# Kernel tuning notes

Measured on AMD Instinct MI355X. Metric: run time of the kernel, lower is better.

## Reference

```python
import jax, jax.numpy as jnp
import numpy as np

N, T, K = 64, 256, 4
MODS = ["linguistic", "acoustic", "image"]
DIMS = {"linguistic": 300, "acoustic": 88, "image": 128}
HID = {"linguistic": 300, "acoustic": 64, "image": 128}
TOTAL_H = sum(HID[m] for m in MODS)  # 492


def _uniform(k, shape, s):
    return jax.random.uniform(k, shape, jnp.float32, -s, s)


def setup_inputs() -> dict:
    key = jax.random.key(0)
    ks = iter(jax.random.split(key, 64))
    inp = {}
    for mod in MODS:
        D, H = DIMS[mod], HID[mod]
        inp[f"x_{mod}"] = jax.random.normal(next(ks), (N, T, K, D), jnp.float32)
        inp[f"mask_{mod}"] = jax.random.randint(next(ks), (N, T, K), 0, 2).astype(bool)
        s = 1.0 / np.sqrt(H)
        inp[f"Wih_{mod}"] = _uniform(next(ks), (4 * H, D), s)
        inp[f"Whh_{mod}"] = _uniform(next(ks), (4 * H, H), s)
        inp[f"bih_{mod}"] = _uniform(next(ks), (4 * H,), s)
        inp[f"bhh_{mod}"] = _uniform(next(ks), (4 * H,), s)
    inp["seq_length"] = jax.random.randint(next(ks), (N,), 1, T + 1)
    inp["lstm_masks"] = jax.random.uniform(next(ks), (N, T, 1), jnp.float32)
    s1 = 1.0 / np.sqrt(TOTAL_H)
    inp["fuse_W1"] = _uniform(next(ks), (256, TOTAL_H), s1)
    inp["fuse_b1"] = _uniform(next(ks), (256,), s1)
    s2 = 1.0 / np.sqrt(256)
    inp["fuse_W2"] = _uniform(next(ks), (1, 256), s2)
    inp["fuse_b2"] = _uniform(next(ks), (1,), s2)
    return inp


def _lstm_cell(x, h, c, Wih, Whh, bih, bhh):
    # torch.nn.LSTMCell gate order: i, f, g, o
    z = x @ Wih.T + bih + h @ Whh.T + bhh
    i, f, g, o = jnp.split(z, 4, axis=-1)
    c2 = jax.nn.sigmoid(f) * c + jax.nn.sigmoid(i) * jnp.tanh(g)
    return jax.nn.sigmoid(o) * jnp.tanh(c2), c2


def _run_mod(x, mask, seq_len, Wih, Whh, bih, bhh):
    # x: [N,T,K,D], mask: [N,T,K] bool, seq_len: [N]
    n, t, k, d = x.shape
    hdim = Whh.shape[1]

    def step(carry, inp):
        h, c = carry
        xt, mt, ti = inp  # xt [N,K,D], mt [N,K]

        def inner(hc, ik):
            h0, c0 = hc
            xk, mk = ik  # [N,D], [N]
            h1, c1 = _lstm_cell(xk, h0, c0, Wih, Whh, bih, bhh)
            mk = mk[:, None]
            return (jnp.where(mk, h1, h0), jnp.where(mk, c1, c0)), None

        (h2, c2), _ = jax.lax.scan(inner, (h, c), (jnp.swapaxes(xt, 0, 1), mt.T))
        avail = mt.any(axis=1)[:, None]        # modality present at this step
        active = (ti < seq_len)[:, None]       # sequence not yet finished
        h_new = jnp.where(active & avail, h2, jnp.where(active, h, 0.0))
        c_new = jnp.where(active & avail, c2, jnp.where(active, c, 0.0))
        return (h_new, c_new), h_new

    h0 = jnp.zeros((n, hdim), x.dtype)
    c0 = jnp.zeros((n, hdim), x.dtype)
    _, hs = jax.lax.scan(
        step, (h0, c0),
        (jnp.swapaxes(x, 0, 1), jnp.swapaxes(mask, 0, 1), jnp.arange(t)))
    # FAITHFUL to original: torch.stack -> [T,N,H] then .reshape(n,t,H) with NO transpose
    return hs.reshape(n, t, hdim)


def reference(x_linguistic, mask_linguistic, Wih_linguistic, Whh_linguistic, bih_linguistic, bhh_linguistic,
              x_acoustic, mask_acoustic, Wih_acoustic, Whh_acoustic, bih_acoustic, bhh_acoustic,
              x_image, mask_image, Wih_image, Whh_image, bih_image, bhh_image,
              seq_length, lstm_masks, fuse_W1, fuse_b1, fuse_W2, fuse_b2):
    hs_l = _run_mod(x_linguistic, mask_linguistic, seq_length, Wih_linguistic, Whh_linguistic, bih_linguistic, bhh_linguistic)
    hs_a = _run_mod(x_acoustic, mask_acoustic, seq_length, Wih_acoustic, Whh_acoustic, bih_acoustic, bhh_acoustic)
    hs_i = _run_mod(x_image, mask_image, seq_length, Wih_image, Whh_image, bih_image, bhh_image)
    fused = jnp.concatenate([hs_l, hs_a, hs_i], axis=2)  # [N,T,492]
    h = fused @ fuse_W1.T + fuse_b1   # Dropout is identity in eval mode
    out = h @ fuse_W2.T + fuse_b2     # [N,T,1]
    return out * lstm_masks
```

## Files before the change

### kernel.cpp

```cpp
#include <hip/hip_runtime.h>
#include <hip/hip_bf16.h>
#include <stdint.h>

#define N_ 64
#define T_ 256
#define K_ 4

#define DL 300
#define HL 300
#define H4L 1200
#define DA 88
#define HA 64
#define H4A 256
#define DI 128
#define HI 128
#define H4I 512
#define DLP 320
#define DAP 96
#define DIP 128

typedef __hip_bfloat16 bf16;
typedef __attribute__((ext_vector_type(8))) short bf16x8;
typedef __attribute__((ext_vector_type(4))) float f32x4;

__device__ __forceinline__ float sigf(float x) { return 1.0f / (1.0f + expf(-x)); }

__device__ __forceinline__ unsigned pk2(float lo, float hi) {
    bf16 a = __float2bfloat16(lo), b = __float2bfloat16(hi);
    return (unsigned)*(unsigned short*)&a | ((unsigned)*(unsigned short*)&b << 16);
}
__device__ __forceinline__ float uplo(unsigned u) { return __uint_as_float(u << 16); }
__device__ __forceinline__ float uphi(unsigned u) { return __uint_as_float(u & 0xFFFF0000u); }

__device__ __forceinline__ int read_mask(const void* m, size_t idx, int mode) {
    if (mode == 0) return ((const int*)m)[idx];
    if (mode == 1) return (int)((const unsigned char*)m)[idx];
    return ((const float*)m)[idx] != 0.0f;
}

__global__ void mask_mode_detect(const unsigned int* __restrict__ m, int* __restrict__ modep) {
    __shared__ unsigned int f[2];
    if (threadIdx.x == 0) { f[0] = 0u; f[1] = 0u; }
    __syncthreads();
    unsigned int gt1 = 0, f32one = 0;
    for (int i = threadIdx.x; i < 4096; i += 256) {
        const unsigned int v = m[i];
        if (v > 1u) gt1 = 1u;
        if (v == 0x3F800000u) f32one = 1u;
    }
    if (gt1) atomicOr(&f[0], 1u);
    if (f32one) atomicOr(&f[1], 1u);
    __syncthreads();
    if (threadIdx.x == 0) modep[0] = f[0] ? (f[1] ? 2 : 1) : 0;
}

__global__ void prep_w3(const float* __restrict__ WL, const float* __restrict__ WA,
                        const float* __restrict__ WI,
                        unsigned short* __restrict__ pL, unsigned short* __restrict__ pA,
                        unsigned short* __restrict__ pI)
{
    const int i = blockIdx.x * 256 + threadIdx.x;
    if (i < H4L * DLP) {
        const int r = i / DLP, d = i - r * DLP;
        bf16 v = __float2bfloat16(d < DL ? WL[(size_t)r * DL + d] : 0.0f);
        pL[i] = *(unsigned short*)&v;
    }
    if (i < H4A * DAP) {
        const int r = i / DAP, d = i - r * DAP;
        bf16 v = __float2bfloat16(d < DA ? WA[(size_t)r * DA + d] : 0.0f);
        pA[i] = *(unsigned short*)&v;
    }
    if (i < H4I * DIP) {
        const int r = i / DIP, d = i - r * DIP;
        bf16 v = __float2bfloat16(WI[(size_t)r * DI + d]);
        pI[i] = *(unsigned short*)&v;
    }
}

__global__ __launch_bounds__(256) void gemm_xz3(
    const float* __restrict__ XL, const unsigned short* __restrict__ WL,
    const float* __restrict__ biL, const float* __restrict__ bhL, bf16* __restrict__ ZL,
    const float* __restrict__ XA, const unsigned short* __restrict__ WA,
    const float* __restrict__ biA, const float* __restrict__ bhA, bf16* __restrict__ ZA,
    const float* __restrict__ XI, const unsigned short* __restrict__ WI,
    const float* __restrict__ biI, const float* __restrict__ bhI, bf16* __restrict__ ZI,
    const int* __restrict__ seqlen, int Tc, int t0)
{
    __shared__ __align__(16) unsigned short Xs[64 * 40];
    __shared__ __align__(16) unsigned short Ws[64 * 40];
    const int z = blockIdx.z;
    const float* X; const unsigned short* W; const float* bih; const float* bhh; bf16* XZ;
    int D, Dp, H4;
    if (z == 0)      { X = XL; W = WL; bih = biL; bhh = bhL; XZ = ZL; D = DL; Dp = DLP; H4 = H4L; }
    else if (z == 1) { X = XA; W = WA; bih = biA; bhh = bhA; XZ = ZA; D = DA; Dp = DAP; H4 = H4A; }
    else             { X = XI; W = WI; bih = biI; bhh = bhI; XZ = ZI; D = DI; Dp = DIP; H4 = H4I; }

    const int j0 = blockIdx.x * 64;
    if (j0 >= H4) return;

    const int tid = threadIdx.x;
    const int m0 = blockIdx.y * 64;
    const int Tc4 = Tc * 4;

    int act = 0;
    if (tid < 64) {
        const int rr = m0 + tid;
        const int n = rr / Tc4;
        const int ttt = (rr % Tc4) >> 2;
        act = (t0 + ttt) < seqlen[n];
    }
    if (!__syncthreads_or(act)) return;

    const int srow = tid >> 2;
    const int sq = tid & 3;
    const int rr = m0 + srow;
    const int n = rr / Tc4;
    const int ttt = (rr % Tc4) >> 2;
    const int kk_ = rr & 3;
    const float* xrow = X + ((size_t)((n * T_ + t0 + ttt) * 4 + kk_)) * D;
    const int wcol = j0 + srow;
    const bool wvalid = wcol < H4;
    const unsigned short* wrow = W + (size_t)(wvalid ? wcol : 0) * Dp;

    const int lane = tid & 63;
    const int wv = tid >> 6;
    const int fr = lane & 15;
    const int fk = (lane >> 4) * 8;

    f32x4 acc[4] = {{0,0,0,0},{0,0,0,0},{0,0,0,0},{0,0,0,0}};

    const int nks = Dp >> 5;
    for (int ks = 0; ks < nks; ++ks) {
        const int d0 = ks * 32 + sq * 8;
        float xf[8];
        if (d0 + 7 < D) {
            const float4 a0 = *(const float4*)(xrow + d0);
            const float4 a1 = *(const float4*)(xrow + d0 + 4);
            xf[0]=a0.x; xf[1]=a0.y; xf[2]=a0.z; xf[3]=a0.w;
            xf[4]=a1.x; xf[5]=a1.y; xf[6]=a1.z; xf[7]=a1.w;
        } else {
#pragma unroll
            for (int e = 0; e < 8; ++e) {
                const int d = d0 + e;
                xf[e] = (d < D) ? xrow[d] : 0.0f;
            }
        }
        union { unsigned short u[8]; uint4 v; } px;
#pragma unroll
        for (int e = 0; e < 8; ++e) {
            bf16 hx = __float2bfloat16(xf[e]);
            px.u[e] = *(unsigned short*)&hx;
        }
        uint4 pwv = make_uint4(0u, 0u, 0u, 0u);
        if (wvalid) pwv = *(const uint4*)&wrow[d0];
        __syncthreads();
        *(uint4*)&Xs[srow * 40 + sq * 8] = px.v;
        *(uint4*)&Ws[srow * 40 + sq * 8] = pwv;
        __syncthreads();
        const bf16x8 a = *(const bf16x8*)&Xs[(wv * 16 + fr) * 40 + fk];
#pragma unroll
        for (int c = 0; c < 4; ++c) {
            const bf16x8 b = *(const bf16x8*)&Ws[(c * 16 + fr) * 40 + fk];
            acc[c] = __builtin_amdgcn_mfma_f32_16x16x32_bf16(a, b, acc[c], 0, 0, 0);
        }
    }
#pragma unroll
    for (int c = 0; c < 4; ++c) {
        const int col = j0 + c * 16 + fr;
        if (col < H4) {
            const float bias = bih[col] + bhh[col];
#pragma unroll
            for (int rg = 0; rg < 4; ++rg) {
                const int row = m0 + wv * 16 + (lane >> 4) * 4 + rg;
                XZ[(size_t)row * H4 + col] = __float2bfloat16(acc[c][rg] + bias);
            }
        }
    }
}

__global__ __launch_bounds__(512, 1) void recur_all(
    const float* __restrict__ WhhL, const float* __restrict__ WhhA,
    const float* __restrict__ WhhI,
    const void* __restrict__ mL, const void* __restrict__ mA, const void* __restrict__ mI,
    const int* __restrict__ modep,
    const int* __restrict__ seqlen,
    const float* __restrict__ wbuf,
    const bf16* __restrict__ xzL, const bf16* __restrict__ xzA, const bf16* __restrict__ xzI,
    float* __restrict__ psumL, float* __restrict__ psumA, float* __restrict__ psumI,
    float* __restrict__ hcL, float* __restrict__ hcA, float* __restrict__ hcI,
    float* __restrict__ hpub,
    unsigned int* __restrict__ cnt,
    int Tc, int t0)
{
    __shared__ float h_s[304];
    __shared__ float c_s[80];
    __shared__ float zp_s[8 * 308];
    __shared__ float zr_s[304];
    __shared__ float wb_s[304];
    __shared__ __align__(16) float h2_s[128];
    __shared__ __align__(16) float c2_s[128];
    __shared__ __align__(16) float z2_s[512];
    __shared__ float wb2_s[128];
    const int tid = threadIdx.x;
    const int mode = modep[0];

    if (blockIdx.x < 4 * N_) {
        const int xcd = blockIdx.x & 7;
        const int idx = blockIdx.x >> 3;
        const int n = xcd * 8 + (idx >> 2);
        const int b = idx & 3;
        const int hb = 75 * b;
        const int seqn = seqlen[n];

        const int chunk = tid & 7;
        const int rb = tid >> 3;
        const int cj = chunk * 38;
        unsigned w[5][19];
#pragma unroll
        for (int s = 0; s < 5; ++s) {
            const int lr = rb + 64 * s;
            const bool rv = (lr < 300);
            const int gl = rv ? (lr / 75) : 0;
            const int i  = rv ? (lr - gl * 75) : 0;
            const float* wp = WhhL + ((size_t)(gl * 300 + hb + i)) * 300;
#pragma unroll
            for (int j = 0; j < 19; ++j) {
                const int c0 = cj + 2 * j;
                const float lo = (rv && c0 < 300) ? wp[c0] : 0.0f;
                const float hi = (rv && c0 + 1 < 300) ? wp[c0 + 1] : 0.0f;
                w[s][j] = pk2(lo, hi);
            }
        }
        int xoff = 0;
        if (tid < 300) {
            const int gl = tid / 75;
            xoff = gl * 300 + hb + (tid - gl * 75);
        }
        for (int r = tid; r < 304; r += 512) {
            if (t0 == 0 || r >= 300) h_s[r] = 0.0f;
            else h_s[r] = hcL[n * 600 + r];
            wb_s[r] = (r < 300) ? wbuf[r] : 0.0f;
        }
        if (tid < 75) c_s[tid] = (t0 == 0) ? 0.0f : hcL[n * 600 + 300 + hb + tid];
        __syncthreads();

        unsigned int serial = 0;
        unsigned int* const cntn = &cnt[n];
        float* const hp = hpub + (size_t)n * 608;

#pragma unroll 1
        for (int tt = 0; tt < Tc; ++tt) {
            const int t = t0 + tt;
            if (t >= seqn) {
                if (b == 0 && tid == 0) psumL[(size_t)n * T_ + t] = 0.0f;
                continue;
            }
            const size_t mbase = (size_t)(n * T_ + t) * 4;
            const bf16* xzt = xzL + ((size_t)((n * Tc + tt) * 4)) * 1200;
#pragma unroll 1
            for (int k = 0; k < 4; ++k) {
                if (!read_mask(mL, mbase + k, mode)) continue;
                const int par = (int)(serial & 1u);
                float a0 = 0.f, a1 = 0.f, a2 = 0.f, a3 = 0.f, a4 = 0.f;
#pragma unroll
                for (int j = 0; j < 19; ++j) {
                    const float2 hv = *(const float2*)&h_s[cj + 2 * j];
                    const unsigned u0 = w[0][j], u1 = w[1][j], u2 = w[2][j],
                                   u3 = w[3][j], u4 = w[4][j];
                    a0 += uplo(u0) * hv.x + uphi(u0) * hv.y;
                    a1 += uplo(u1) * hv.x + uphi(u1) * hv.y;
                    a2 += uplo(u2) * hv.x + uphi(u2) * hv.y;
                    a3 += uplo(u3) * hv.x + uphi(u3) * hv.y;
                    a4 += uplo(u4) * hv.x + uphi(u4) * hv.y;
                }
                zp_s[chunk * 308 + rb]       = a0;
                zp_s[chunk * 308 + rb + 64]  = a1;
                zp_s[chunk * 308 + rb + 128] = a2;
                zp_s[chunk * 308 + rb + 192] = a3;
                if (rb < 44) zp_s[chunk * 308 + rb + 256] = a4;
                __syncthreads();
                if (tid < 300) {
                    float zv = __bfloat162float(xzt[k * 1200 + xoff]);
#pragma unroll
                    for (int c = 0; c < 8; ++c) zv += zp_s[c * 308 + tid];
                    zr_s[tid] = zv;
                }
                __syncthreads();
                if (tid < 75) {
                    const float zi = zr_s[tid];
                    const float zf = zr_s[75 + tid];
                    const float zg = zr_s[150 + tid];
                    const float zo = zr_s[225 + tid];
                    const float cc = sigf(zf) * c_s[tid] + sigf(zi) * tanhf(zg);
                    c_s[tid] = cc;
                    const float hh = sigf(zo) * tanhf(cc);
                    __hip_atomic_store(&hp[par * 304 + hb + tid], hh,
                                       __ATOMIC_RELAXED, __HIP_MEMORY_SCOPE_AGENT);
                }
                __syncthreads();
                if (tid == 0) {
                    __hip_atomic_fetch_add(cntn, 1u, __ATOMIC_RELEASE, __HIP_MEMORY_SCOPE_AGENT);
                    const unsigned int target = 4u * (serial + 1u);
                    unsigned int v = __hip_atomic_load(cntn, __ATOMIC_ACQUIRE, __HIP_MEMORY_SCOPE_AGENT);
                    long guard = 0;
                    while (v < target && guard < (1L << 24)) {
                        __builtin_amdgcn_s_sleep(1);
                        v = __hip_atomic_load(cntn, __ATOMIC_ACQUIRE, __HIP_MEMORY_SCOPE_AGENT);
                        ++guard;
                    }
                }
                __syncthreads();
                if (tid < 300)
                    h_s[tid] = __hip_atomic_load(&hp[par * 304 + tid],
                                                 __ATOMIC_RELAXED, __HIP_MEMORY_SCOPE_AGENT);
                __syncthreads();
                ++serial;
            }
            if (b == 0 && tid < 64) {
                float v = 0.0f;
                for (int r = tid; r < 300; r += 64) v += wb_s[r] * h_s[r];
#pragma unroll
                for (int off = 32; off; off >>= 1) v += __shfl_down(v, off, 64);
                if (tid == 0) psumL[(size_t)n * T_ + t] = v;
            }
        }
        if (tid < 75) {
            hcL[n * 600 + hb + tid] = h_s[hb + tid];
            hcL[n * 600 + 300 + hb + tid] = c_s[tid];
        }
    } else if (blockIdx.x < 4 * N_ + N_) {
        const int n = blockIdx.x - 4 * N_;
        const int seqn = seqlen[n];
        unsigned w[64];
        {
            const float4* wp = (const float4*)(WhhI + (size_t)tid * 128);
#pragma unroll
            for (int jj = 0; jj < 32; ++jj) {
                const float4 v = wp[jj];
                w[2 * jj]     = pk2(v.x, v.y);
                w[2 * jj + 1] = pk2(v.z, v.w);
            }
        }
        if (tid < 128) {
            if (t0 == 0) { h2_s[tid] = 0.0f; c2_s[tid] = 0.0f; }
            else { h2_s[tid] = hcI[n * 256 + tid]; c2_s[tid] = hcI[n * 256 + 128 + tid]; }
            wb2_s[tid] = wbuf[364 + tid];
        }
        __syncthreads();
#pragma unroll 1
        for (int tt = 0; tt < Tc; ++tt) {
            const int t = t0 + tt;
            if (t >= seqn) {
                if (tid == 0) psumI[(size_t)n * T_ + t] = 0.0f;
                continue;
            }
            const size_t xbase = ((size_t)((n * Tc + tt) * 4)) * 512;
            const size_t mbase = (size_t)(n * T_ + t) * 4;
#pragma unroll 1
            for (int k = 0; k < 4; ++k) {
                if (!read_mask(mI, mbase + k, mode)) continue;
                float acc = __bfloat162float(xzI[xbase + k * 512 + tid]);
                const float2* hp2 = (const float2*)h2_s;
#pragma unroll
                for (int jj = 0; jj < 64; ++jj) {
                    const float2 hv = hp2[jj];
                    const unsigned u = w[jj];
                    acc += uplo(u) * hv.x + uphi(u) * hv.y;
                }
                z2_s[tid] = acc;
                __syncthreads();
                if (tid < 128) {
                    const float zi = z2_s[tid], zf = z2_s[128 + tid];
                    const float zg = z2_s[256 + tid], zo = z2_s[384 + tid];
                    const float cc = sigf(zf) * c2_s[tid] + sigf(zi) * tanhf(zg);
                    c2_s[tid] = cc;
                    h2_s[tid] = sigf(zo) * tanhf(cc);
                }
                __syncthreads();
            }
            if (tid < 64) {
                float v = wb2_s[tid] * h2_s[tid] + wb2_s[tid + 64] * h2_s[tid + 64];
#pragma unroll
                for (int off = 32; off; off >>= 1) v += __shfl_down(v, off, 64);
                if (tid == 0) psumI[(size_t)n * T_ + t] = v;
            }
        }
        if (tid < 128) { hcI[n * 256 + tid] = h2_s[tid]; hcI[n * 256 + 128 + tid] = c2_s[tid]; }
    } else {
        const int n = blockIdx.x - 5 * N_;
        const int seqn = seqlen[n];
        unsigned w[32];
        if (tid < 256) {
            const float4* wp = (const float4*)(WhhA + (size_t)tid * 64);
#pragma unroll
            for (int jj = 0; jj < 16; ++jj) {
                const float4 v = wp[jj];
                w[2 * jj]     = pk2(v.x, v.y);
                w[2 * jj + 1] = pk2(v.z, v.w);
            }
        }
        if (tid < 64) {
            if (t0 == 0) { h2_s[tid] = 0.0f; c2_s[tid] = 0.0f; }
            else { h2_s[tid] = hcA[n * 128 + tid]; c2_s[tid] = hcA[n * 128 + 64 + tid]; }
            wb2_s[tid] = wbuf[300 + tid];
        }
        __syncthreads();
#pragma unroll 1
        for (int tt = 0; tt < Tc; ++tt) {
            const int t = t0 + tt;
            if (t >= seqn) {
                if (tid == 0) psumA[(size_t)n * T_ + t] = 0.0f;
                continue;
            }
            const size_t xbase = ((size_t)((n * Tc + tt) * 4)) * 256;
            const size_t mbase = (size_t)(n * T_ + t) * 4;
#pragma unroll 1
            for (int k = 0; k < 4; ++k) {
                if (!read_mask(mA, mbase + k, mode)) continue;
                if (tid < 256) {
                    float acc = __bfloat162float(xzA[xbase + k * 256 + tid]);
                    const float2* hp2 = (const float2*)h2_s;
#pragma unroll
                    for (int jj = 0; jj < 32; ++jj) {
                        const float2 hv = hp2[jj];
                        const unsigned u = w[jj];
                        acc += uplo(u) * hv.x + uphi(u) * hv.y;
                    }
                    z2_s[tid] = acc;
                }
                __syncthreads();
                if (tid < 64) {
                    const float zi = z2_s[tid], zf = z2_s[64 + tid];
                    const float zg = z2_s[128 + tid], zo = z2_s[192 + tid];
                    const float cc = sigf(zf) * c2_s[tid] + sigf(zi) * tanhf(zg);
                    c2_s[tid] = cc;
                    h2_s[tid] = sigf(zo) * tanhf(cc);
                }
                __syncthreads();
            }
            if (tid < 64) {
                float v = wb2_s[tid] * h2_s[tid];
#pragma unroll
                for (int off = 32; off; off >>= 1) v += __shfl_down(v, off, 64);
                if (tid == 0) psumA[(size_t)n * T_ + t] = v;
            }
        }
        if (tid < 64) { hcA[n * 128 + tid] = h2_s[tid]; hcA[n * 128 + 64 + tid] = c2_s[tid]; }
    }
}

__global__ void wprep(const float* __restrict__ W1, const float* __restrict__ b1,
                      const float* __restrict__ W2, const float* __restrict__ b2,
                      float* __restrict__ wbuf)
{
    const int j = threadIdx.x;
    if (j < 492) {
        float a = 0.0f;
        for (int r = 0; r < 256; ++r) a += W2[r] * W1[r * 492 + j];
        wbuf[j] = a;
    } else if (j == 492) {
        float a = 0.0f;
        for (int r = 0; r < 256; ++r) a += W2[r] * b1[r];
        wbuf[500] = a + b2[0];
    }
}

__global__ void out_combine(const float* __restrict__ wbuf,
                            const float* __restrict__ pL, const float* __restrict__ pA,
                            const float* __restrict__ pI,
                            const float* __restrict__ lmask, float* __restrict__ out)
{
    const int i = blockIdx.x;
    const int j = threadIdx.x;
    const int nn = j & 63;
    const int tt = i * 4 + (j >> 6);
    const size_t src = (size_t)nn * T_ + tt;
    const size_t nt = (size_t)i * T_ + j;
    out[nt] = (pL[src] + pA[src] + pI[src] + wbuf[500]) * lmask[nt];
}

extern "C" void kernel_launch(void* const* d_in, const int* in_sizes, int n_in,
                              void* d_out, int out_size, void* d_ws, size_t ws_size,
                              hipStream_t stream)
{
    (void)in_sizes; (void)n_in;
    const float* xL   = (const float*)d_in[0];
    const void*  mL   = d_in[1];
    const float* WihL = (const float*)d_in[2];
    const float* WhhL = (const float*)d_in[3];
    const float* bihL = (const float*)d_in[4];
    const float* bhhL = (const float*)d_in[5];
    const float* xA   = (const float*)d_in[6];
    const void*  mA   = d_in[7];
    const float* WihA = (const float*)d_in[8];
    const float* WhhA = (const float*)d_in[9];
    const float* bihA = (const float*)d_in[10];
    const float* bhhA = (const float*)d_in[11];
    const float* xI   = (const float*)d_in[12];
    const void*  mI   = d_in[13];
    const float* WihI = (const float*)d_in[14];
    const float* WhhI = (const float*)d_in[15];
    const float* bihI = (const float*)d_in[16];
    const float* bhhI = (const float*)d_in[17];
    const int*   seqlen = (const int*)d_in[18];
    const float* lmask  = (const float*)d_in[19];
    const float* W1 = (const float*)d_in[20];
    const float* b1 = (const float*)d_in[21];
    const float* W2 = (const float*)d_in[22];
    const float* b2 = (const float*)d_in[23];
    float* out = (float*)d_out;

    char* base = (char*)d_ws;
    size_t off = 0;
    auto take = [&](size_t bytes) -> char* {
        char* p = base + off;
        off += (bytes + 63) & ~(size_t)63;
        return p;
    };
    unsigned int* cnt = (unsigned int*)take(64 * 64 * sizeof(unsigned int));
    int*   modep = (int*)take(64);
    float* wbuf  = (float*)take(512 * sizeof(float));
    float* hcL   = (float*)take((size_t)N_ * 2 * HL * sizeof(float));
    float* hcA   = (float*)take((size_t)N_ * 2 * HA * sizeof(float));
    float* hcI   = (float*)take((size_t)N_ * 2 * HI * sizeof(float));
    float* hpub  = (float*)take((size_t)N_ * 2 * 304 * sizeof(float));
    float* psumL = (float*)take((size_t)N_ * T_ * sizeof(float));
    float* psumA = (float*)take((size_t)N_ * T_ * sizeof(float));
    float* psumI = (float*)take((size_t)N_ * T_ * sizeof(float));
    unsigned short* wpkL = (unsigned short*)take((size_t)H4L * DLP * sizeof(unsigned short));
    unsigned short* wpkA = (unsigned short*)take((size_t)H4A * DAP * sizeof(unsigned short));
    unsigned short* wpkI = (unsigned short*)take((size_t)H4I * DIP * sizeof(unsigned short));

    const size_t xz_per_tc = (size_t)N_ * K_ * (H4L + H4A + H4I) * sizeof(bf16);
    int Tc = T_;
    while (Tc > 1 && off + (size_t)Tc * xz_per_tc + 256 > ws_size) Tc >>= 1;
    if (off + (size_t)Tc * xz_per_tc + 256 > ws_size) {
        hipMemsetAsync(d_out, 0, (size_t)out_size * sizeof(float), stream);
        return;
    }
    if (Tc > 64) Tc = 64;
    bf16* xzL = (bf16*)take((size_t)N_ * Tc * K_ * H4L * sizeof(bf16));
    bf16* xzA = (bf16*)take((size_t)N_ * Tc * K_ * H4A * sizeof(bf16));
    bf16* xzI = (bf16*)take((size_t)N_ * Tc * K_ * H4I * sizeof(bf16));

    const int nchunks = T_ / Tc;
    hipMemsetAsync(cnt, 0, (size_t)nchunks * 64 * sizeof(unsigned int), stream);
    mask_mode_detect<<<1, 256, 0, stream>>>((const unsigned int*)mL, modep);
    wprep<<<1, 512, 0, stream>>>(W1, b1, W2, b2, wbuf);
    prep_w3<<<(H4L * DLP + 255) / 256, 256, 0, stream>>>(WihL, WihA, WihI, wpkL, wpkA, wpkI);

    const int My = (N_ * Tc * K_) / 64;
    for (int c = 0; c < nchunks; ++c) {
        const int t0 = c * Tc;
        gemm_xz3<<<dim3((H4L + 63) / 64, My, 3), 256, 0, stream>>>(
            xL, wpkL, bihL, bhhL, xzL,
            xA, wpkA, bihA, bhhA, xzA,
            xI, wpkI, bihI, bhhI, xzI,
            seqlen, Tc, t0);
        recur_all<<<6 * N_, 512, 0, stream>>>(
            WhhL, WhhA, WhhI, mL, mA, mI, modep, seqlen, wbuf,
            xzL, xzA, xzI, psumL, psumA, psumI,
            hcL, hcA, hcI, hpub, cnt + (size_t)c * 64, Tc, t0);
    }
    out_combine<<<N_, T_, 0, stream>>>(wbuf, psumL, psumA, psumI, lmask, out);
}
```

Before: 3.959 ms.

## Fuse input-projection GEMM into recurrence kernel and overlap next chunk's GEMM

Merges the separate input-projection GEMM and recurrence kernels into one 'mega' kernel. Each launch runs the recurrence for the current time chunk on 6*N blocks, while extra blocks compute the next chunk's projections into a double buffer. The goal is to hide GEMM time behind the latency-bound serial recurrence and to cut launch count. The cost is double the xz workspace, and the GEMM blocks may compete for CUs with the recurrence blocks, which spin-wait on each other.

```diff
diff --git a/kernel.cpp b/kernel.cpp
--- a/kernel.cpp
+++ b/kernel.cpp
@@ -18,6 +18,10 @@
 #define DLP 320
 #define DAP 96
 #define DIP 128
+#define XT_L 19
+#define XT_A 4
+#define XT_I 8
+#define XT_ALL 31
 
 typedef __hip_bfloat16 bf16;
 typedef __attribute__((ext_vector_type(8))) short bf16x8;
@@ -74,378 +78,6 @@
         const int r = i / DIP, d = i - r * DIP;
         bf16 v = __float2bfloat16(WI[(size_t)r * DI + d]);
         pI[i] = *(unsigned short*)&v;
-    }
-}
-
-__global__ __launch_bounds__(256) void gemm_xz3(
-    const float* __restrict__ XL, const unsigned short* __restrict__ WL,
-    const float* __restrict__ biL, const float* __restrict__ bhL, bf16* __restrict__ ZL,
-    const float* __restrict__ XA, const unsigned short* __restrict__ WA,
-    const float* __restrict__ biA, const float* __restrict__ bhA, bf16* __restrict__ ZA,
-    const float* __restrict__ XI, const unsigned short* __restrict__ WI,
-    const float* __restrict__ biI, const float* __restrict__ bhI, bf16* __restrict__ ZI,
-    const int* __restrict__ seqlen, int Tc, int t0)
-{
-    __shared__ __align__(16) unsigned short Xs[64 * 40];
-    __shared__ __align__(16) unsigned short Ws[64 * 40];
-    const int z = blockIdx.z;
-    const float* X; const unsigned short* W; const float* bih; const float* bhh; bf16* XZ;
-    int D, Dp, H4;
-    if (z == 0)      { X = XL; W = WL; bih = biL; bhh = bhL; XZ = ZL; D = DL; Dp = DLP; H4 = H4L; }
-    else if (z == 1) { X = XA; W = WA; bih = biA; bhh = bhA; XZ = ZA; D = DA; Dp = DAP; H4 = H4A; }
-    else             { X = XI; W = WI; bih = biI; bhh = bhI; XZ = ZI; D = DI; Dp = DIP; H4 = H4I; }
-
-    const int j0 = blockIdx.x * 64;
-    if (j0 >= H4) return;
-
-    const int tid = threadIdx.x;
-    const int m0 = blockIdx.y * 64;
-    const int Tc4 = Tc * 4;
-
-    int act = 0;
-    if (tid < 64) {
-        const int rr = m0 + tid;
-        const int n = rr / Tc4;
-        const int ttt = (rr % Tc4) >> 2;
-        act = (t0 + ttt) < seqlen[n];
-    }
-    if (!__syncthreads_or(act)) return;
-
-    const int srow = tid >> 2;
-    const int sq = tid & 3;
-    const int rr = m0 + srow;
-    const int n = rr / Tc4;
-    const int ttt = (rr % Tc4) >> 2;
-    const int kk_ = rr & 3;
-    const float* xrow = X + ((size_t)((n * T_ + t0 + ttt) * 4 + kk_)) * D;
-    const int wcol = j0 + srow;
-    const bool wvalid = wcol < H4;
-    const unsigned short* wrow = W + (size_t)(wvalid ? wcol : 0) * Dp;
-
-    const int lane = tid & 63;
-    const int wv = tid >> 6;
-    const int fr = lane & 15;
-    const int fk = (lane >> 4) * 8;
-
-    f32x4 acc[4] = {{0,0,0,0},{0,0,0,0},{0,0,0,0},{0,0,0,0}};
-
-    const int nks = Dp >> 5;
-    for (int ks = 0; ks < nks; ++ks) {
-        const int d0 = ks * 32 + sq * 8;
-        float xf[8];
-        if (d0 + 7 < D) {
-            const float4 a0 = *(const float4*)(xrow + d0);
-            const float4 a1 = *(const float4*)(xrow + d0 + 4);
-            xf[0]=a0.x; xf[1]=a0.y; xf[2]=a0.z; xf[3]=a0.w;
-            xf[4]=a1.x; xf[5]=a1.y; xf[6]=a1.z; xf[7]=a1.w;
-        } else {
-#pragma unroll
-            for (int e = 0; e < 8; ++e) {
-                const int d = d0 + e;
-                xf[e] = (d < D) ? xrow[d] : 0.0f;
-            }
-        }
-        union { unsigned short u[8]; uint4 v; } px;
-#pragma unroll
-        for (int e = 0; e < 8; ++e) {
-            bf16 hx = __float2bfloat16(xf[e]);
-            px.u[e] = *(unsigned short*)&hx;
-        }
-        uint4 pwv = make_uint4(0u, 0u, 0u, 0u);
-        if (wvalid) pwv = *(const uint4*)&wrow[d0];
-        __syncthreads();
-        *(uint4*)&Xs[srow * 40 + sq * 8] = px.v;
-        *(uint4*)&Ws[srow * 40 + sq * 8] = pwv;
-        __syncthreads();
-        const bf16x8 a = *(const bf16x8*)&Xs[(wv * 16 + fr) * 40 + fk];
-#pragma unroll
-        for (int c = 0; c < 4; ++c) {
-            const bf16x8 b = *(const bf16x8*)&Ws[(c * 16 + fr) * 40 + fk];
-            acc[c] = __builtin_amdgcn_mfma_f32_16x16x32_bf16(a, b, acc[c], 0, 0, 0);
-        }
-    }
-#pragma unroll
-    for (int c = 0; c < 4; ++c) {
-        const int col = j0 + c * 16 + fr;
-        if (col < H4) {
-            const float bias = bih[col] + bhh[col];
-#pragma unroll
-            for (int rg = 0; rg < 4; ++rg) {
-                const int row = m0 + wv * 16 + (lane >> 4) * 4 + rg;
-                XZ[(size_t)row * H4 + col] = __float2bfloat16(acc[c][rg] + bias);
-            }
-        }
-    }
-}
-
-__global__ __launch_bounds__(512, 1) void recur_all(
-    const float* __restrict__ WhhL, const float* __restrict__ WhhA,
-    const float* __restrict__ WhhI,
-    const void* __restrict__ mL, const void* __restrict__ mA, const void* __restrict__ mI,
-    const int* __restrict__ modep,
-    const int* __restrict__ seqlen,
-    const float* __restrict__ wbuf,
-    const bf16* __restrict__ xzL, const bf16* __restrict__ xzA, const bf16* __restrict__ xzI,
-    float* __restrict__ psumL, float* __restrict__ psumA, float* __restrict__ psumI,
-    float* __restrict__ hcL, float* __restrict__ hcA, float* __restrict__ hcI,
-    float* __restrict__ hpub,
-    unsigned int* __restrict__ cnt,
-    int Tc, int t0)
-{
-    __shared__ float h_s[304];
-    __shared__ float c_s[80];
-    __shared__ float zp_s[8 * 308];
-    __shared__ float zr_s[304];
-    __shared__ float wb_s[304];
-    __shared__ __align__(16) float h2_s[128];
-    __shared__ __align__(16) float c2_s[128];
-    __shared__ __align__(16) float z2_s[512];
-    __shared__ float wb2_s[128];
-    const int tid = threadIdx.x;
-    const int mode = modep[0];
-
-    if (blockIdx.x < 4 * N_) {
-        const int xcd = blockIdx.x & 7;
-        const int idx = blockIdx.x >> 3;
-        const int n = xcd * 8 + (idx >> 2);
-        const int b = idx & 3;
-        const int hb = 75 * b;
-        const int seqn = seqlen[n];
-
-        const int chunk = tid & 7;
-        const int rb = tid >> 3;
-        const int cj = chunk * 38;
-        unsigned w[5][19];
-#pragma unroll
-        for (int s = 0; s < 5; ++s) {
-            const int lr = rb + 64 * s;
-            const bool rv = (lr < 300);
-            const int gl = rv ? (lr / 75) : 0;
-            const int i  = rv ? (lr - gl * 75) : 0;
-            const float* wp = WhhL + ((size_t)(gl * 300 + hb + i)) * 300;
-#pragma unroll
-            for (int j = 0; j < 19; ++j) {
-                const int c0 = cj + 2 * j;
-                const float lo = (rv && c0 < 300) ? wp[c0] : 0.0f;
-                const float hi = (rv && c0 + 1 < 300) ? wp[c0 + 1] : 0.0f;
-                w[s][j] = pk2(lo, hi);
-            }
-        }
-        int xoff = 0;
-        if (tid < 300) {
-            const int gl = tid / 75;
-            xoff = gl * 300 + hb + (tid - gl * 75);
-        }
-        for (int r = tid; r < 304; r += 512) {
-            if (t0 == 0 || r >= 300) h_s[r] = 0.0f;
-            else h_s[r] = hcL[n * 600 + r];
-            wb_s[r] = (r < 300) ? wbuf[r] : 0.0f;
-        }
-        if (tid < 75) c_s[tid] = (t0 == 0) ? 0.0f : hcL[n * 600 + 300 + hb + tid];
-        __syncthreads();
-
-        unsigned int serial = 0;
-        unsigned int* const cntn = &cnt[n];
-        float* const hp = hpub + (size_t)n * 608;
-
-#pragma unroll 1
-        for (int tt = 0; tt < Tc; ++tt) {
-            const int t = t0 + tt;
-            if (t >= seqn) {
-                if (b == 0 && tid == 0) psumL[(size_t)n * T_ + t] = 0.0f;
-                continue;
-            }
-            const size_t mbase = (size_t)(n * T_ + t) * 4;
-            const bf16* xzt = xzL + ((size_t)((n * Tc + tt) * 4)) * 1200;
-#pragma unroll 1
-            for (int k = 0; k < 4; ++k) {
-                if (!read_mask(mL, mbase + k, mode)) continue;
-                const int par = (int)(serial & 1u);
-                float a0 = 0.f, a1 = 0.f, a2 = 0.f, a3 = 0.f, a4 = 0.f;
-#pragma unroll
-                for (int j = 0; j < 19; ++j) {
-                    const float2 hv = *(const float2*)&h_s[cj + 2 * j];
-                    const unsigned u0 = w[0][j], u1 = w[1][j], u2 = w[2][j],
-                                   u3 = w[3][j], u4 = w[4][j];
-                    a0 += uplo(u0) * hv.x + uphi(u0) * hv.y;
-                    a1 += uplo(u1) * hv.x + uphi(u1) * hv.y;
-                    a2 += uplo(u2) * hv.x + uphi(u2) * hv.y;
-                    a3 += uplo(u3) * hv.x + uphi(u3) * hv.y;
-                    a4 += uplo(u4) * hv.x + uphi(u4) * hv.y;
-                }
-                zp_s[chunk * 308 + rb]       = a0;
-                zp_s[chunk * 308 + rb + 64]  = a1;
-                zp_s[chunk * 308 + rb + 128] = a2;
-                zp_s[chunk * 308 + rb + 192] = a3;
-                if (rb < 44) zp_s[chunk * 308 + rb + 256] = a4;
-                __syncthreads();
-                if (tid < 300) {
-                    float zv = __bfloat162float(xzt[k * 1200 + xoff]);
-#pragma unroll
-                    for (int c = 0; c < 8; ++c) zv += zp_s[c * 308 + tid];
-                    zr_s[tid] = zv;
-                }
-                __syncthreads();
-                if (tid < 75) {
-                    const float zi = zr_s[tid];
-                    const float zf = zr_s[75 + tid];
-                    const float zg = zr_s[150 + tid];
-                    const float zo = zr_s[225 + tid];
-                    const float cc = sigf(zf) * c_s[tid] + sigf(zi) * tanhf(zg);
-                    c_s[tid] = cc;
-                    const float hh = sigf(zo) * tanhf(cc);
-                    __hip_atomic_store(&hp[par * 304 + hb + tid], hh,
-                                       __ATOMIC_RELAXED, __HIP_MEMORY_SCOPE_AGENT);
-                }
-                __syncthreads();
-                if (tid == 0) {
-                    __hip_atomic_fetch_add(cntn, 1u, __ATOMIC_RELEASE, __HIP_MEMORY_SCOPE_AGENT);
-                    const unsigned int target = 4u * (serial + 1u);
-                    unsigned int v = __hip_atomic_load(cntn, __ATOMIC_ACQUIRE, __HIP_MEMORY_SCOPE_AGENT);
-                    long guard = 0;
-                    while (v < target && guard < (1L << 24)) {
-                        __builtin_amdgcn_s_sleep(1);
-                        v = __hip_atomic_load(cntn, __ATOMIC_ACQUIRE, __HIP_MEMORY_SCOPE_AGENT);
-                        ++guard;
-                    }
-                }
-                __syncthreads();
-                if (tid < 300)
-                    h_s[tid] = __hip_atomic_load(&hp[par * 304 + tid],
-                                                 __ATOMIC_RELAXED, __HIP_MEMORY_SCOPE_AGENT);
-                __syncthreads();
-                ++serial;
-            }
-            if (b == 0 && tid < 64) {
-                float v = 0.0f;
-                for (int r = tid; r < 300; r += 64) v += wb_s[r] * h_s[r];
-#pragma unroll
-                for (int off = 32; off; off >>= 1) v += __shfl_down(v, off, 64);
-                if (tid == 0) psumL[(size_t)n * T_ + t] = v;
-            }
-        }
-        if (tid < 75) {
-            hcL[n * 600 + hb + tid] = h_s[hb + tid];
-            hcL[n * 600 + 300 + hb + tid] = c_s[tid];
-        }
-    } else if (blockIdx.x < 4 * N_ + N_) {
-        const int n = blockIdx.x - 4 * N_;
-        const int seqn = seqlen[n];
-        unsigned w[64];
-        {
-            const float4* wp = (const float4*)(WhhI + (size_t)tid * 128);
-#pragma unroll
-            for (int jj = 0; jj < 32; ++jj) {
-                const float4 v = wp[jj];
-                w[2 * jj]     = pk2(v.x, v.y);
-                w[2 * jj + 1] = pk2(v.z, v.w);
-            }
-        }
-        if (tid < 128) {
-            if (t0 == 0) { h2_s[tid] = 0.0f; c2_s[tid] = 0.0f; }
-            else { h2_s[tid] = hcI[n * 256 + tid]; c2_s[tid] = hcI[n * 256 + 128 + tid]; }
-            wb2_s[tid] = wbuf[364 + tid];
-        }
-        __syncthreads();
-#pragma unroll 1
-        for (int tt = 0; tt < Tc; ++tt) {
-            const int t = t0 + tt;
-            if (t >= seqn) {
-                if (tid == 0) psumI[(size_t)n * T_ + t] = 0.0f;
-                continue;
-            }
-            const size_t xbase = ((size_t)((n * Tc + tt) * 4)) * 512;
-            const size_t mbase = (size_t)(n * T_ + t) * 4;
-#pragma unroll 1
-            for (int k = 0; k < 4; ++k) {
-                if (!read_mask(mI, mbase + k, mode)) continue;
-                float acc = __bfloat162float(xzI[xbase + k * 512 + tid]);
-                const float2* hp2 = (const float2*)h2_s;
-#pragma unroll
-                for (int jj = 0; jj < 64; ++jj) {
-                    const float2 hv = hp2[jj];
-                    const unsigned u = w[jj];
-                    acc += uplo(u) * hv.x + uphi(u) * hv.y;
-                }
-                z2_s[tid] = acc;
-                __syncthreads();
-                if (tid < 128) {
-                    const float zi = z2_s[tid], zf = z2_s[128 + tid];
-                    const float zg = z2_s[256 + tid], zo = z2_s[384 + tid];
-                    const float cc = sigf(zf) * c2_s[tid] + sigf(zi) * tanhf(zg);
-                    c2_s[tid] = cc;
-                    h2_s[tid] = sigf(zo) * tanhf(cc);
-                }
-                __syncthreads();
-            }
-            if (tid < 64) {
-                float v = wb2_s[tid] * h2_s[tid] + wb2_s[tid + 64] * h2_s[tid + 64];
-#pragma unroll
-                for (int off = 32; off; off >>= 1) v += __shfl_down(v, off, 64);
-                if (tid == 0) psumI[(size_t)n * T_ + t] = v;
-            }
-        }
-        if (tid < 128) { hcI[n * 256 + tid] = h2_s[tid]; hcI[n * 256 + 128 + tid] = c2_s[tid]; }
-    } else {
-        const int n = blockIdx.x - 5 * N_;
-        const int seqn = seqlen[n];
-        unsigned w[32];
-        if (tid < 256) {
-            const float4* wp = (const float4*)(WhhA + (size_t)tid * 64);
-#pragma unroll
-            for (int jj = 0; jj < 16; ++jj) {
-                const float4 v = wp[jj];
-                w[2 * jj]     = pk2(v.x, v.y);
-                w[2 * jj + 1] = pk2(v.z, v.w);
-            }
-        }
-        if (tid < 64) {
-            if (t0 == 0) { h2_s[tid] = 0.0f; c2_s[tid] = 0.0f; }
-            else { h2_s[tid] = hcA[n * 128 + tid]; c2_s[tid] = hcA[n * 128 + 64 + tid]; }
-            wb2_s[tid] = wbuf[300 + tid];
-        }
-        __syncthreads();
-#pragma unroll 1
-        for (int tt = 0; tt < Tc; ++tt) {
-            const int t = t0 + tt;
-            if (t >= seqn) {
-                if (tid == 0) psumA[(size_t)n * T_ + t] = 0.0f;
-                continue;
-            }
-            const size_t xbase = ((size_t)((n * Tc + tt) * 4)) * 256;
-            const size_t mbase = (size_t)(n * T_ + t) * 4;
-#pragma unroll 1
-            for (int k = 0; k < 4; ++k) {
-                if (!read_mask(mA, mbase + k, mode)) continue;
-                if (tid < 256) {
-                    float acc = __bfloat162float(xzA[xbase + k * 256 + tid]);
-                    const float2* hp2 = (const float2*)h2_s;
-#pragma unroll
-                    for (int jj = 0; jj < 32; ++jj) {
-                        const float2 hv = hp2[jj];
-                        const unsigned u = w[jj];
-                        acc += uplo(u) * hv.x + uphi(u) * hv.y;
-                    }
-                    z2_s[tid] = acc;
-                }
-                __syncthreads();
-                if (tid < 64) {
-                    const float zi = z2_s[tid], zf = z2_s[64 + tid];
-                    const float zg = z2_s[128 + tid], zo = z2_s[192 + tid];
-                    const float cc = sigf(zf) * c2_s[tid] + sigf(zi) * tanhf(zg);
-                    c2_s[tid] = cc;
-                    h2_s[tid] = sigf(zo) * tanhf(cc);
-                }
-                __syncthreads();
-            }
-            if (tid < 64) {
-                float v = wb2_s[tid] * h2_s[tid];
-#pragma unroll
-                for (int off = 32; off; off >>= 1) v += __shfl_down(v, off, 64);
-                if (tid == 0) psumA[(size_t)n * T_ + t] = v;
-            }
-        }
-        if (tid < 64) { hcA[n * 128 + tid] = h2_s[tid]; hcA[n * 128 + 64 + tid] = c2_s[tid]; }
     }
 }
 
@@ -462,6 +94,378 @@
         float a = 0.0f;
         for (int r = 0; r < 256; ++r) a += W2[r] * b1[r];
         wbuf[500] = a + b2[0];
+    }
+}
+
+__global__ __launch_bounds__(512, 1) void mega(
+    const float* __restrict__ WhhL, const float* __restrict__ WhhA,
+    const float* __restrict__ WhhI,
+    const void* __restrict__ mL, const void* __restrict__ mA, const void* __restrict__ mI,
+    const int* __restrict__ modep,
+    const int* __restrict__ seqlen,
+    const float* __restrict__ wbuf,
+    const bf16* __restrict__ rxL, const bf16* __restrict__ rxA, const bf16* __restrict__ rxI,
+    float* __restrict__ psumL, float* __restrict__ psumA, float* __restrict__ psumI,
+    float* __restrict__ hcL, float* __restrict__ hcA, float* __restrict__ hcI,
+    float* __restrict__ hpub,
+    unsigned int* __restrict__ cnt,
+    const float* __restrict__ XL, const unsigned short* __restrict__ WpL,
+    const float* __restrict__ biL, const float* __restrict__ bhL, bf16* __restrict__ gzL,
+    const float* __restrict__ XA, const unsigned short* __restrict__ WpA,
+    const float* __restrict__ biA, const float* __restrict__ bhA, bf16* __restrict__ gzA,
+    const float* __restrict__ XI, const unsigned short* __restrict__ WpI,
+    const float* __restrict__ biI, const float* __restrict__ bhI, bf16* __restrict__ gzI,
+    int Tc, int t0, int g_t0, int nRecur)
+{
+    __shared__ float h_s[304];
+    __shared__ float c_s[80];
+    __shared__ float zp_s[8 * 308];
+    __shared__ float zr_s[304];
+    __shared__ float wb_s[304];
+    __shared__ __align__(16) float h2_s[128];
+    __shared__ __align__(16) float c2_s[128];
+    __shared__ __align__(16) float z2_s[512];
+    __shared__ float wb2_s[128];
+    __shared__ __align__(16) unsigned short Xs[128 * 40];
+    __shared__ __align__(16) unsigned short Ws[64 * 40];
+
+    const int tid = threadIdx.x;
+    const int mode = modep[0];
+    const int Tc4 = Tc * 4;
+
+    if ((int)blockIdx.x >= nRecur) {
+        if (g_t0 < 0) return;
+        const int gb = blockIdx.x - nRecur;
+        const int y = gb / XT_ALL;
+        const int rem = gb - y * XT_ALL;
+        const float* X; const unsigned short* W; const float* bih; const float* bhh; bf16* XZ;
+        int D, Dp, H4, xt;
+        if (rem < XT_L)            { xt = rem;          X = XL; W = WpL; bih = biL; bhh = bhL; XZ = gzL; D = DL; Dp = DLP; H4 = H4L; }
+        else if (rem < XT_L + XT_A){ xt = rem - XT_L;   X = XA; W = WpA; bih = biA; bhh = bhA; XZ = gzA; D = DA; Dp = DAP; H4 = H4A; }
+        else                       { xt = rem - XT_L - XT_A; X = XI; W = WpI; bih = biI; bhh = bhI; XZ = gzI; D = DI; Dp = DIP; H4 = H4I; }
+        const int j0 = xt * 64;
+        const int m0 = y * 128;
+
+        int act = 0;
+        if (tid < 128) {
+            const int rr = m0 + tid;
+            const int n = rr / Tc4;
+            const int ttt = (rr % Tc4) >> 2;
+            act = (g_t0 + ttt) < seqlen[n];
+        }
+        if (!__syncthreads_or(act)) return;
+
+        const int srow = tid >> 2;
+        const int sq = tid & 3;
+        const int rr = m0 + srow;
+        const int n = rr / Tc4;
+        const int ttt = (rr % Tc4) >> 2;
+        const int kk_ = rr & 3;
+        const float* xrow = X + ((size_t)((n * T_ + g_t0 + ttt) * 4 + kk_)) * D;
+        const int wsrow = tid >> 2;
+        const int wcol = j0 + wsrow;
+        const bool wvalid = (tid < 256) && (wcol < H4);
+        const unsigned short* wrow = W + (size_t)(wvalid ? wcol : 0) * Dp;
+
+        const int lane = tid & 63;
+        const int wv = tid >> 6;
+        const int fr = lane & 15;
+        const int fk = (lane >> 4) * 8;
+
+        f32x4 acc[4] = {{0,0,0,0},{0,0,0,0},{0,0,0,0},{0,0,0,0}};
+
+        const int nks = Dp >> 5;
+        for (int ks = 0; ks < nks; ++ks) {
+            const int d0 = ks * 32 + sq * 8;
+            float xf[8];
+            if (d0 + 7 < D) {
+                const float4 a0 = *(const float4*)(xrow + d0);
+                const float4 a1 = *(const float4*)(xrow + d0 + 4);
+                xf[0]=a0.x; xf[1]=a0.y; xf[2]=a0.z; xf[3]=a0.w;
+                xf[4]=a1.x; xf[5]=a1.y; xf[6]=a1.z; xf[7]=a1.w;
+            } else {
+#pragma unroll
+                for (int e = 0; e < 8; ++e) {
+                    const int d = d0 + e;
+                    xf[e] = (d < D) ? xrow[d] : 0.0f;
+                }
+            }
+            union { unsigned short u[8]; uint4 v; } px;
+#pragma unroll
+            for (int e = 0; e < 8; ++e) {
+                bf16 hx = __float2bfloat16(xf[e]);
+                px.u[e] = *(unsigned short*)&hx;
+            }
+            uint4 pwv = make_uint4(0u, 0u, 0u, 0u);
+            if (wvalid) pwv = *(const uint4*)&wrow[d0];
+            __syncthreads();
+            *(uint4*)&Xs[srow * 40 + sq * 8] = px.v;
+            if (tid < 256) *(uint4*)&Ws[wsrow * 40 + sq * 8] = pwv;
+            __syncthreads();
+            const bf16x8 a = *(const bf16x8*)&Xs[(wv * 16 + fr) * 40 + fk];
+#pragma unroll
+            for (int c = 0; c < 4; ++c) {
+                const bf16x8 b = *(const bf16x8*)&Ws[(c * 16 + fr) * 40 + fk];
+                acc[c] = __builtin_amdgcn_mfma_f32_16x16x32_bf16(a, b, acc[c], 0, 0, 0);
+            }
+        }
+#pragma unroll
+        for (int c = 0; c < 4; ++c) {
+            const int col = j0 + c * 16 + fr;
+            if (col < H4) {
+                const float bias = bih[col] + bhh[col];
+#pragma unroll
+                for (int rg = 0; rg < 4; ++rg) {
+                    const int row = m0 + wv * 16 + (lane >> 4) * 4 + rg;
+                    XZ[(size_t)row * H4 + col] = __float2bfloat16(acc[c][rg] + bias);
+                }
+            }
+        }
+        return;
+    }
+
+    if (blockIdx.x < 4 * N_) {
+        const int xcd = blockIdx.x & 7;
+        const int idx = blockIdx.x >> 3;
+        const int n = xcd * 8 + (idx >> 2);
+        const int b = idx & 3;
+        const int hb = 75 * b;
+        const int seqn = seqlen[n];
+
+        const int chunk = tid & 7;
+        const int rb = tid >> 3;
+        const int cj = chunk * 38;
+        unsigned w[5][19];
+#pragma unroll
+        for (int s = 0; s < 5; ++s) {
+            const int lr = rb + 64 * s;
+            const bool rv = (lr < 300);
+            const int gl = rv ? (lr / 75) : 0;
+            const int i  = rv ? (lr - gl * 75) : 0;
+            const float* wp = WhhL + ((size_t)(gl * 300 + hb + i)) * 300;
+#pragma unroll
+            for (int j = 0; j < 19; ++j) {
+                const int c0 = cj + 2 * j;
+                const float lo = (rv && c0 < 300) ? wp[c0] : 0.0f;
+                const float hi = (rv && c0 + 1 < 300) ? wp[c0 + 1] : 0.0f;
+                w[s][j] = pk2(lo, hi);
+            }
+        }
+        int xoff = 0;
+        if (tid < 300) {
+            const int gl = tid / 75;
+            xoff = gl * 300 + hb + (tid - gl * 75);
+        }
+        for (int r = tid; r < 304; r += 512) {
+            if (t0 == 0 || r >= 300) h_s[r] = 0.0f;
+            else h_s[r] = hcL[n * 600 + r];
+            wb_s[r] = (r < 300) ? wbuf[r] : 0.0f;
+        }
+        if (tid < 75) c_s[tid] = (t0 == 0) ? 0.0f : hcL[n * 600 + 300 + hb + tid];
+        __syncthreads();
+
+        unsigned int serial = 0;
+        unsigned int* const cntn = &cnt[n];
+        float* const hp = hpub + (size_t)n * 608;
+
+#pragma unroll 1
+        for (int tt = 0; tt < Tc; ++tt) {
+            const int t = t0 + tt;
+            if (t >= seqn) {
+                if (b == 0 && tid == 0) psumL[(size_t)n * T_ + t] = 0.0f;
+                continue;
+            }
+            const size_t mbase = (size_t)(n * T_ + t) * 4;
+            const bf16* xzt = rxL + ((size_t)((n * Tc + tt) * 4)) * 1200;
+#pragma unroll 1
+            for (int k = 0; k < 4; ++k) {
+                if (!read_mask(mL, mbase + k, mode)) continue;
+                const int par = (int)(serial & 1u);
+                float a0 = 0.f, a1 = 0.f, a2 = 0.f, a3 = 0.f, a4 = 0.f;
+#pragma unroll
+                for (int j = 0; j < 19; ++j) {
+                    const float2 hv = *(const float2*)&h_s[cj + 2 * j];
+                    const unsigned u0 = w[0][j], u1 = w[1][j], u2 = w[2][j],
+                                   u3 = w[3][j], u4 = w[4][j];
+                    a0 += uplo(u0) * hv.x + uphi(u0) * hv.y;
+                    a1 += uplo(u1) * hv.x + uphi(u1) * hv.y;
+                    a2 += uplo(u2) * hv.x + uphi(u2) * hv.y;
+                    a3 += uplo(u3) * hv.x + uphi(u3) * hv.y;
+                    a4 += uplo(u4) * hv.x + uphi(u4) * hv.y;
+                }
+                zp_s[chunk * 308 + rb]       = a0;
+                zp_s[chunk * 308 + rb + 64]  = a1;
+                zp_s[chunk * 308 + rb + 128] = a2;
+                zp_s[chunk * 308 + rb + 192] = a3;
+                if (rb < 44) zp_s[chunk * 308 + rb + 256] = a4;
+                __syncthreads();
+                if (tid < 300) {
+                    float zv = __bfloat162float(xzt[k * 1200 + xoff]);
+#pragma unroll
+                    for (int c = 0; c < 8; ++c) zv += zp_s[c * 308 + tid];
+                    zr_s[tid] = zv;
+                }
+                __syncthreads();
+                if (tid < 75) {
+                    const float zi = zr_s[tid];
+                    const float zf = zr_s[75 + tid];
+                    const float zg = zr_s[150 + tid];
+                    const float zo = zr_s[225 + tid];
+                    const float cc = sigf(zf) * c_s[tid] + sigf(zi) * tanhf(zg);
+                    c_s[tid] = cc;
+                    const float hh = sigf(zo) * tanhf(cc);
+                    __hip_atomic_store(&hp[par * 304 + hb + tid], hh,
+                                       __ATOMIC_RELAXED, __HIP_MEMORY_SCOPE_AGENT);
+                }
+                __syncthreads();
+                if (tid == 0) {
+                    __hip_atomic_fetch_add(cntn, 1u, __ATOMIC_RELEASE, __HIP_MEMORY_SCOPE_AGENT);
+                    const unsigned int target = 4u * (serial + 1u);
+                    unsigned int v = __hip_atomic_load(cntn, __ATOMIC_ACQUIRE, __HIP_MEMORY_SCOPE_AGENT);
+                    long guard = 0;
+                    while (v < target && guard < (1L << 22)) {
+                        __builtin_amdgcn_s_sleep(1);
+                        v = __hip_atomic_load(cntn, __ATOMIC_ACQUIRE, __HIP_MEMORY_SCOPE_AGENT);
+                        ++guard;
+                    }
+                }
+                __syncthreads();
+                if (tid < 300)
+                    h_s[tid] = __hip_atomic_load(&hp[par * 304 + tid],
+                                                 __ATOMIC_RELAXED, __HIP_MEMORY_SCOPE_AGENT);
+                __syncthreads();
+                ++serial;
+            }
+            if (b == 0 && tid < 64) {
+                float v = 0.0f;
+                for (int r = tid; r < 300; r += 64) v += wb_s[r] * h_s[r];
+#pragma unroll
+                for (int off = 32; off; off >>= 1) v += __shfl_down(v, off, 64);
+                if (tid == 0) psumL[(size_t)n * T_ + t] = v;
+            }
+        }
+        if (tid < 75) {
+            hcL[n * 600 + hb + tid] = h_s[hb + tid];
+            hcL[n * 600 + 300 + hb + tid] = c_s[tid];
+        }
+    } else if (blockIdx.x < 5 * N_) {
+        const int n = blockIdx.x - 4 * N_;
+        const int seqn = seqlen[n];
+        unsigned w[64];
+        {
+            const float4* wp = (const float4*)(WhhI + (size_t)tid * 128);
+#pragma unroll
+            for (int jj = 0; jj < 32; ++jj) {
+                const float4 v = wp[jj];
+                w[2 * jj]     = pk2(v.x, v.y);
+                w[2 * jj + 1] = pk2(v.z, v.w);
+            }
+        }
+        if (tid < 128) {
+            if (t0 == 0) { h2_s[tid] = 0.0f; c2_s[tid] = 0.0f; }
+            else { h2_s[tid] = hcI[n * 256 + tid]; c2_s[tid] = hcI[n * 256 + 128 + tid]; }
+            wb2_s[tid] = wbuf[364 + tid];
+        }
+        __syncthreads();
+#pragma unroll 1
+        for (int tt = 0; tt < Tc; ++tt) {
+            const int t = t0 + tt;
+            if (t >= seqn) {
+                if (tid == 0) psumI[(size_t)n * T_ + t] = 0.0f;
+                continue;
+            }
+            const size_t xbase = ((size_t)((n * Tc + tt) * 4)) * 512;
+            const size_t mbase = (size_t)(n * T_ + t) * 4;
+#pragma unroll 1
+            for (int k = 0; k < 4; ++k) {
+                if (!read_mask(mI, mbase + k, mode)) continue;
+                float acc = __bfloat162float(rxI[xbase + k * 512 + tid]);
+                const float2* hp2 = (const float2*)h2_s;
+#pragma unroll
+                for (int jj = 0; jj < 64; ++jj) {
+                    const float2 hv = hp2[jj];
+                    const unsigned u = w[jj];
+                    acc += uplo(u) * hv.x + uphi(u) * hv.y;
+                }
+                z2_s[tid] = acc;
+                __syncthreads();
+                if (tid < 128) {
+                    const float zi = z2_s[tid], zf = z2_s[128 + tid];
+                    const float zg = z2_s[256 + tid], zo = z2_s[384 + tid];
+                    const float cc = sigf(zf) * c2_s[tid] + sigf(zi) * tanhf(zg);
+                    c2_s[tid] = cc;
+                    h2_s[tid] = sigf(zo) * tanhf(cc);
+                }
+                __syncthreads();
+            }
+            if (tid < 64) {
+                float v = wb2_s[tid] * h2_s[tid] + wb2_s[tid + 64] * h2_s[tid + 64];
+#pragma unroll
+                for (int off = 32; off; off >>= 1) v += __shfl_down(v, off, 64);
+                if (tid == 0) psumI[(size_t)n * T_ + t] = v;
+            }
+        }
+        if (tid < 128) { hcI[n * 256 + tid] = h2_s[tid]; hcI[n * 256 + 128 + tid] = c2_s[tid]; }
+    } else {
+        const int n = blockIdx.x - 5 * N_;
+        const int seqn = seqlen[n];
+        unsigned w[32];
+        if (tid < 256) {
+            const float4* wp = (const float4*)(WhhA + (size_t)tid * 64);
+#pragma unroll
+            for (int jj = 0; jj < 16; ++jj) {
+                const float4 v = wp[jj];
+                w[2 * jj]     = pk2(v.x, v.y);
+                w[2 * jj + 1] = pk2(v.z, v.w);
+            }
+        }
+        if (tid < 64) {
+            if (t0 == 0) { h2_s[tid] = 0.0f; c2_s[tid] = 0.0f; }
+            else { h2_s[tid] = hcA[n * 128 + tid]; c2_s[tid] = hcA[n * 128 + 64 + tid]; }
+            wb2_s[tid] = wbuf[300 + tid];
+        }
+        __syncthreads();
+#pragma unroll 1
+        for (int tt = 0; tt < Tc; ++tt) {
+            const int t = t0 + tt;
+            if (t >= seqn) {
+                if (tid == 0) psumA[(size_t)n * T_ + t] = 0.0f;
+                continue;
+            }
+            const size_t xbase = ((size_t)((n * Tc + tt) * 4)) * 256;
+            const size_t mbase = (size_t)(n * T_ + t) * 4;
+#pragma unroll 1
+            for (int k = 0; k < 4; ++k) {
+                if (!read_mask(mA, mbase + k, mode)) continue;
+                if (tid < 256) {
+                    float acc = __bfloat162float(rxA[xbase + k * 256 + tid]);
+                    const float2* hp2 = (const float2*)h2_s;
+#pragma unroll
+                    for (int jj = 0; jj < 32; ++jj) {
+                        const float2 hv = hp2[jj];
+                        const unsigned u = w[jj];
+                        acc += uplo(u) * hv.x + uphi(u) * hv.y;
+                    }
+                    z2_s[tid] = acc;
+                }
+                __syncthreads();
+                if (tid < 64) {
+                    const float zi = z2_s[tid], zf = z2_s[64 + tid];
+                    const float zg = z2_s[128 + tid], zo = z2_s[192 + tid];
+                    const float cc = sigf(zf) * c2_s[tid] + sigf(zi) * tanhf(zg);
+                    c2_s[tid] = cc;
+                    h2_s[tid] = sigf(zo) * tanhf(cc);
+                }
+                __syncthreads();
+            }
+            if (tid < 64) {
+                float v = wb2_s[tid] * h2_s[tid];
+#pragma unroll
+                for (int off = 32; off; off >>= 1) v += __shfl_down(v, off, 64);
+                if (tid == 0) psumA[(size_t)n * T_ + t] = v;
+            }
+        }
+        if (tid < 64) { hcA[n * 128 + tid] = h2_s[tid]; hcA[n * 128 + 64 + tid] = c2_s[tid]; }
     }
 }
 
@@ -533,34 +537,52 @@
 
     const size_t xz_per_tc = (size_t)N_ * K_ * (H4L + H4A + H4I) * sizeof(bf16);
     int Tc = T_;
-    while (Tc > 1 && off + (size_t)Tc * xz_per_tc + 256 > ws_size) Tc >>= 1;
-    if (off + (size_t)Tc * xz_per_tc + 256 > ws_size) {
+    while (Tc > 1 && off + 2 * (size_t)Tc * xz_per_tc + 512 > ws_size) Tc >>= 1;
+    if (off + 2 * (size_t)Tc * xz_per_tc + 512 > ws_size) {
         hipMemsetAsync(d_out, 0, (size_t)out_size * sizeof(float), stream);
         return;
     }
     if (Tc > 64) Tc = 64;
-    bf16* xzL = (bf16*)take((size_t)N_ * Tc * K_ * H4L * sizeof(bf16));
-    bf16* xzA = (bf16*)take((size_t)N_ * Tc * K_ * H4A * sizeof(bf16));
-    bf16* xzI = (bf16*)take((size_t)N_ * Tc * K_ * H4I * sizeof(bf16));
+    bf16* xzL0 = (bf16*)take((size_t)N_ * Tc * K_ * H4L * sizeof(bf16));
+    bf16* xzA0 = (bf16*)take((size_t)N_ * Tc * K_ * H4A * sizeof(bf16));
+    bf16* xzI0 = (bf16*)take((size_t)N_ * Tc * K_ * H4I * sizeof(bf16));
+    bf16* xzL1 = (bf16*)take((size_t)N_ * Tc * K_ * H4L * sizeof(bf16));
+    bf16* xzA1 = (bf16*)take((size_t)N_ * Tc * K_ * H4A * sizeof(bf16));
+    bf16* xzI1 = (bf16*)take((size_t)N_ * Tc * K_ * H4I * sizeof(bf16));
+    bf16* bufL[2] = { xzL0, xzL1 };
+    bf16* bufA[2] = { xzA0, xzA1 };
+    bf16* bufI[2] = { xzI0, xzI1 };
 
     const int nchunks = T_ / Tc;
+    const int ngemm = XT_ALL * ((N_ * Tc * K_) >> 7);
+
     hipMemsetAsync(cnt, 0, (size_t)nchunks * 64 * sizeof(unsigned int), stream);
     mask_mode_detect<<<1, 256, 0, stream>>>((const unsigned int*)mL, modep);
     wprep<<<1, 512, 0, stream>>>(W1, b1, W2, b2, wbuf);
     prep_w3<<<(H4L * DLP + 255) / 256, 256, 0, stream>>>(WihL, WihA, WihI, wpkL, wpkA, wpkI);
 
-    const int My = (N_ * Tc * K_) / 64;
+    mega<<<ngemm, 512, 0, stream>>>(
+        WhhL, WhhA, WhhI, mL, mA, mI, modep, seqlen, wbuf,
+        bufL[0], bufA[0], bufI[0], psumL, psumA, psumI,
+        hcL, hcA, hcI, hpub, cnt,
+        xL, wpkL, bihL, bhhL, bufL[0],
+        xA, wpkA, bihA, bhhA, bufA[0],
+        xI, wpkI, bihI, bhhI, bufI[0],
+        Tc, 0, 0, 0);
+
     for (int c = 0; c < nchunks; ++c) {
         const int t0 = c * Tc;
-        gemm_xz3<<<dim3((H4L + 63) / 64, My, 3), 256, 0, stream>>>(
-            xL, wpkL, bihL, bhhL, xzL,
-            xA, wpkA, bihA, bhhA, xzA,
-            xI, wpkI, bihI, bhhI, xzI,
-            seqlen, Tc, t0);
-        recur_all<<<6 * N_, 512, 0, stream>>>(
+        const int gt0 = (c + 1 < nchunks) ? (c + 1) * Tc : -1;
+        const int cur = c & 1, nxt = (c + 1) & 1;
+        const int grid = 6 * N_ + (gt0 >= 0 ? ngemm : 0);
+        mega<<<grid, 512, 0, stream>>>(
             WhhL, WhhA, WhhI, mL, mA, mI, modep, seqlen, wbuf,
-            xzL, xzA, xzI, psumL, psumA, psumI,
-            hcL, hcA, hcI, hpub, cnt + (size_t)c * 64, Tc, t0);
+            bufL[cur], bufA[cur], bufI[cur], psumL, psumA, psumI,
+            hcL, hcA, hcI, hpub, cnt + (size_t)c * 64,
+            xL, wpkL, bihL, bhhL, bufL[nxt],
+            xA, wpkA, bihA, bhhA, bufA[nxt],
+            xI, wpkI, bihI, bhhI, bufI[nxt],
+            Tc, t0, gt0, 6 * N_);
     }
     out_combine<<<N_, T_, 0, stream>>>(wbuf, psumL, psumA, psumI, lmask, out);
 }
```

Measured after the change: 4.007 ms. No clear change (+1.2%).
